# Optimization experiments

Hardware: AMD Instinct MI355X
Metric: run time of the kernel (lower is better)

Reference implementation:

```python
import jax, jax.numpy as jnp
import numpy as np
from jax.scipy.linalg import expm

S = 64          # alphabet size (codons)
M = 8           # number of models, prod(model_shape)
N_LEAVES = 32   # leaves of the balanced binary tree
N_EDGES = 62    # nodes 0..62, every non-root node has one parent edge (edge id == child node id)
B = 1024        # batch (alignment columns)
# per-level ranges of child-node ids; node 32+j has children (2j, 2j+1), etc.
LEVELS = [(0, 32), (32, 48), (48, 56), (56, 60), (60, 62)]


def inv_stereographic_projection(p):
    # maps R^{s-1} -> unit sphere S^{s-1}
    n2 = jnp.sum(p * p, axis=-1, keepdims=True)
    return jnp.concatenate([2.0 * p / (n2 + 1.0), (n2 - 1.0) / (n2 + 1.0)], axis=-1)


def generator(R, pi):
    # R: (M, s(s-1)/2) exchangeabilities, pi: (M, s) stationary distribution
    iu, ju = np.triu_indices(S, 1)
    A = jnp.zeros((M, S, S), R.dtype).at[:, iu, ju].set(R).at[:, ju, iu].set(R)
    Q = A * pi[:, None, :]                       # Q_ij = A_ij * pi_j (off-diagonal)
    row = jnp.sum(Q, axis=-1)                    # (M, S)
    return Q - jnp.eye(S, dtype=Q.dtype) * row[:, :, None]


def felsenstein(leave_configuration, R_inv, pi_inv, lengths):
    pi = inv_stereographic_projection(pi_inv) ** 2           # (M, S), rows sum to 1
    R = jnp.exp(R_inv)                                       # positive rates
    Q = generator(R, pi)                                     # (M, S, S)
    tQ = lengths[:, None, None, None] * Q[None]              # (E, M, S, S)
    P = jax.vmap(expm)(tQ.reshape(-1, S, S)).reshape(N_EDGES, M, S, S)
    # leaf alphas: tile leaf observations over the M models -> (n_leaves, B, M, S)
    prev = jnp.broadcast_to(
        leave_configuration.transpose(1, 0, 2)[:, :, None, :],
        (N_LEAVES, leave_configuration.shape[0], M, S))
    # level-synchronous pruning: messages up each parent edge, then product of the two children
    for a, b in LEVELS:
        msg = jnp.einsum('emcd,ebmd->ebmc', P[a:b], prev)    # per-edge transition
        prev = msg[0::2] * msg[1::2]                         # combine sibling pairs
    root = prev[0]                                           # (B, M, S)
    out = jnp.einsum('bms,ms->bm', root, pi)                 # P(data | model m)
    return out.reshape(out.shape[0], M)                      # (B, *model_shape)


def setup_inputs() -> dict:
    key = jax.random.key(0)
    k1, k2, k3, k4 = jax.random.split(key, 4)
    leave_configuration = jax.random.uniform(k1, (B, N_LEAVES, S), dtype=jnp.float32)
    tree_indices = jnp.zeros((B,), dtype=jnp.int32)          # single tree (F=1)
    R_inv = jax.random.uniform(k2, (M, S * (S - 1) // 2), dtype=jnp.float32,
                               minval=-1.0, maxval=1.0)
    pi_inv = jnp.full((M, S - 1), 1.0 / (np.sqrt(S) - 1.0), dtype=jnp.float32) \
        + 0.01 * jax.random.normal(k3, (M, S - 1), dtype=jnp.float32)
    lengths = jax.random.uniform(k4, (N_EDGES,), dtype=jnp.float32,
                                 minval=0.05, maxval=0.5)
    return {'leave_configuration': leave_configuration, 'R_inv': R_inv,
            'pi_inv': pi_inv, 'lengths': lengths, 'tree_indices': tree_indices}


def reference(leave_configuration, R_inv, pi_inv, lengths, tree_indices):
    # F=1: tf.dynamic_partition/gather_nd batch slicing is the identity, so
    # tree_indices is closed over / unused.
    return felsenstein(leave_configuration, R_inv, pi_inv, lengths)
```

## Files before the change

### kernel.cpp

```cpp
#include <hip/hip_runtime.h>

typedef unsigned short u16;
typedef unsigned int u32;
typedef __attribute__((ext_vector_type(8))) __bf16 bf16x8;
typedef __attribute__((ext_vector_type(4))) float f32x4;

constexpr int NM = 8;

constexpr size_t OFF_QP  = 0;
constexpr size_t OFF_PI  = 393216;
constexpr size_t OFF_PBH = 393728;
constexpr size_t OFF_PBL = OFF_PBH + 1015808;

union FR { uint4 u; bf16x8 v; };

__device__ __forceinline__ void split_bf16(float x, u16& h, u16& l) {
  u32 b = __float_as_uint(x);
  u32 hb = (b + 0x7fffu + ((b >> 16) & 1u)) & 0xffff0000u;
  h = (u16)(hb >> 16);
  float r = x - __uint_as_float(hb);
  l = (u16)(__float_as_uint(r) >> 16);
}

__device__ __forceinline__ void split8(const f32x4 a, const f32x4 b,
                                       uint4& hi, uint4& lo) {
  u16 h[8], l[8];
  split_bf16(a.x, h[0], l[0]); split_bf16(a.y, h[1], l[1]);
  split_bf16(a.z, h[2], l[2]); split_bf16(a.w, h[3], l[3]);
  split_bf16(b.x, h[4], l[4]); split_bf16(b.y, h[5], l[5]);
  split_bf16(b.z, h[6], l[6]); split_bf16(b.w, h[7], l[7]);
  hi.x = h[0] | ((u32)h[1] << 16); hi.y = h[2] | ((u32)h[3] << 16);
  hi.z = h[4] | ((u32)h[5] << 16); hi.w = h[6] | ((u32)h[7] << 16);
  lo.x = l[0] | ((u32)l[1] << 16); lo.y = l[2] | ((u32)l[3] << 16);
  lo.z = l[4] | ((u32)l[5] << 16); lo.w = l[6] | ((u32)l[7] << 16);
}

__device__ __forceinline__ void mfma3(f32x4& a, const uint4 ah, const uint4 al,
                                      const uint4 bh, const uint4 bl) {
  FR Ah, Al, Bh, Bl;
  Ah.u = ah; Al.u = al; Bh.u = bh; Bl.u = bl;
  a = __builtin_amdgcn_mfma_f32_16x16x32_bf16(Ah.v, Bh.v, a, 0, 0, 0);
  a = __builtin_amdgcn_mfma_f32_16x16x32_bf16(Ah.v, Bl.v, a, 0, 0, 0);
  a = __builtin_amdgcn_mfma_f32_16x16x32_bf16(Al.v, Bh.v, a, 0, 0, 0);
}

__device__ __forceinline__ void xt_read2(const u32* b, int row, int chunk,
                                         uint4& hi, uint4& lo) {
  const int dw = (row << 5) + (((chunk + row) & 7) << 2);
  hi = *(const uint4*)&b[dw];
  lo = *(const uint4*)&b[2048 + dw];
}
__device__ __forceinline__ void xt_write4(u32* b, int row, int cp, int half,
                                          const f32x4 v) {
  u16 h[4], l[4];
  split_bf16(v.x, h[0], l[0]); split_bf16(v.y, h[1], l[1]);
  split_bf16(v.z, h[2], l[2]); split_bf16(v.w, h[3], l[3]);
  const int dw = (row << 5) + (((cp + row) & 7) << 2) + half * 2;
  uint2 hh, ll;
  hh.x = h[0] | ((u32)h[1] << 16); hh.y = h[2] | ((u32)h[3] << 16);
  ll.x = l[0] | ((u32)l[1] << 16); ll.y = l[2] | ((u32)l[3] << 16);
  *(uint2*)&b[dw] = hh;
  *(uint2*)&b[2048 + dw] = ll;
}

__device__ void mmP(const u32* RX, const u32* CY, u32* dstC, u32* dstR,
                    float* __restrict__ g, int stid) {
  const int ln = stid & 15, kq = (stid >> 4) & 3, ct = stid >> 6;
  const f32x4 z = {0.f, 0.f, 0.f, 0.f};
  uint4 ah[2], al[2];
  #pragma unroll
  for (int kh = 0; kh < 2; ++kh)
    xt_read2(RX, ct * 16 + ln, kh * 4 + kq, ah[kh], al[kh]);
  f32x4 acc[4];
  #pragma unroll
  for (int bt = 0; bt < 4; ++bt) {
    acc[bt] = z;
    #pragma unroll
    for (int kh = 0; kh < 2; ++kh) {
      uint4 bh, bl;
      xt_read2(CY, bt * 16 + ln, kh * 4 + kq, bh, bl);
      mfma3(acc[bt], ah[kh], al[kh], bh, bl);
    }
  }
  #pragma unroll
  for (int bt = 0; bt < 4; ++bt) {
    #pragma unroll
    for (int r = 0; r < 4; ++r)
      g[(ct * 16 + kq * 4 + r) * 64 + bt * 16 + ln] = acc[bt][r];
    if (dstC) xt_write4(dstC, bt * 16 + ln, 2 * ct + (kq >> 1), kq & 1, acc[bt]);
  }
  if (dstR) {
    #pragma unroll
    for (int kh = 0; kh < 2; ++kh)
      xt_read2(CY, ct * 16 + ln, kh * 4 + kq, ah[kh], al[kh]);
    #pragma unroll
    for (int bt = 0; bt < 4; ++bt) {
      f32x4 a2 = z;
      #pragma unroll
      for (int kh = 0; kh < 2; ++kh) {
        uint4 bh, bl;
        xt_read2(RX, bt * 16 + ln, kh * 4 + kq, bh, bl);
        mfma3(a2, ah[kh], al[kh], bh, bl);
      }
      xt_write4(dstR, bt * 16 + ln, 2 * ct + (kq >> 1), kq & 1, a2);
    }
  }
}

__global__ __launch_bounds__(1024) void k_power(const float* __restrict__ R_inv,
                                                const float* __restrict__ pi_inv,
                                                float* __restrict__ ws) {
  const int m = blockIdx.x;
  const int tid = threadIdx.x;
  __shared__ float pis[64];
  __shared__ float n2s;
  __shared__ __align__(16) float Qs[64 * 68];
  __shared__ __align__(16) u32 PB[8][4096];
  if (tid < 64) {
    float p = (tid < 63) ? pi_inv[m * 63 + tid] : 0.f;
    float v = p * p;
    #pragma unroll
    for (int off = 32; off; off >>= 1) v += __shfl_down(v, off, 64);
    if (tid == 0) n2s = v;
  }
  __syncthreads();
  if (tid < 64) {
    const float den = n2s + 1.f;
    const float x = (tid < 63) ? 2.f * pi_inv[m * 63 + tid] / den
                               : (n2s - 1.f) / den;
    const float pv = x * x;
    pis[tid] = pv;
    ws[OFF_PI + (size_t)m * 64 + tid] = pv;
  }
  __syncthreads();
  for (int idx = tid; idx < 4096; idx += 1024) {
    const int i = idx >> 6, j = idx & 63;
    float q = 0.f;
    if (i != j) {
      const int a = min(i, j), b = max(i, j);
      const int kk = a * (127 - a) / 2 + (b - a - 1);
      q = expf(R_inv[m * 2016 + kk]) * pis[j];
    }
    Qs[i * 68 + j] = q;
  }
  __syncthreads();
  if (tid < 64) {
    float s = 0.f;
    #pragma unroll 4
    for (int j4 = 0; j4 < 64; j4 += 4) {
      const f32x4 q = *(const f32x4*)&Qs[tid * 68 + j4];
      s += q.x + q.y + q.z + q.w;
    }
    Qs[tid * 68 + tid] = -s;
  }
  __syncthreads();
  float* g1 = ws + OFF_QP + (size_t)m * 12 * 4096;
  for (int idx = tid; idx < 4096; idx += 1024)
    g1[idx] = Qs[(idx >> 6) * 68 + (idx & 63)];
  if (tid < 512) {
    const int i = tid >> 3, c = tid & 7;
    const f32x4 a = *(const f32x4*)&Qs[i * 68 + c * 8];
    const f32x4 b = *(const f32x4*)&Qs[i * 68 + c * 8 + 4];
    uint4 h, l;
    split8(a, b, h, l);
    const int dw = (i << 5) + (((c + i) & 7) << 2);
    *(uint4*)&PB[0][dw] = h;
    *(uint4*)&PB[0][2048 + dw] = l;
  } else {
    const int t2 = tid - 512, j = t2 >> 3, c = t2 & 7;
    f32x4 a, b;
    a.x = Qs[(c * 8 + 0) * 68 + j]; a.y = Qs[(c * 8 + 1) * 68 + j];
    a.z = Qs[(c * 8 + 2) * 68 + j]; a.w = Qs[(c * 8 + 3) * 68 + j];
    b.x = Qs[(c * 8 + 4) * 68 + j]; b.y = Qs[(c * 8 + 5) * 68 + j];
    b.z = Qs[(c * 8 + 6) * 68 + j]; b.w = Qs[(c * 8 + 7) * 68 + j];
    uint4 h, l;
    split8(a, b, h, l);
    const int dw = (j << 5) + (((c + j) & 7) << 2);
    *(uint4*)&PB[4][dw] = h;
    *(uint4*)&PB[4][2048 + dw] = l;
  }
  __syncthreads();
  const int sub = tid >> 8, stid = tid & 255;
  if (sub == 0) mmP(PB[0], PB[4], PB[5], PB[1], g1 + 4096, stid);
  __syncthreads();
  if (sub == 0) mmP(PB[1], PB[4], PB[6], nullptr, g1 + 2 * 4096, stid);
  else if (sub == 1) mmP(PB[1], PB[5], PB[7], PB[2], g1 + 3 * 4096, stid);
  __syncthreads();
  if (sub == 0) mmP(PB[2], PB[4], nullptr, nullptr, g1 + 4 * 4096, stid);
  else if (sub == 1) mmP(PB[2], PB[5], nullptr, nullptr, g1 + 5 * 4096, stid);
  else if (sub == 2) mmP(PB[2], PB[6], nullptr, nullptr, g1 + 6 * 4096, stid);
  else mmP(PB[2], PB[7], nullptr, PB[3], g1 + 7 * 4096, stid);
  __syncthreads();
  if (sub == 0) mmP(PB[3], PB[4], nullptr, nullptr, g1 + 8 * 4096, stid);
  else if (sub == 1) mmP(PB[3], PB[5], nullptr, nullptr, g1 + 9 * 4096, stid);
  else if (sub == 2) mmP(PB[3], PB[6], nullptr, nullptr, g1 + 10 * 4096, stid);
  else mmP(PB[3], PB[7], nullptr, nullptr, g1 + 11 * 4096, stid);
}

__global__ __launch_bounds__(256) void k_comb(const float* __restrict__ lengths,
                                              const float* __restrict__ ws,
                                              u16* __restrict__ ph_g,
                                              u16* __restrict__ pl_g) {
  const int e = blockIdx.x, m = blockIdx.y, tid = threadIdx.x;
  const float t = lengths[e];
  const float* qp = ws + OFF_QP + (size_t)m * 12 * 4096;
  u16* ph = ph_g + (((size_t)e * 8 + m) << 12);
  u16* pl = pl_g + (((size_t)e * 8 + m) << 12);
  float cf[12];
  cf[0] = t;
  #pragma unroll
  for (int k = 2; k <= 12; ++k) cf[k - 1] = cf[k - 2] * t / (float)k;
  #pragma unroll
  for (int rr = 0; rr < 4; ++rr) {
    const int off = rr * 1024 + tid * 4;
    const int i = off >> 6, j0 = off & 63;
    f32x4 a = {0.f, 0.f, 0.f, 0.f};
    if (i >= j0 && i < j0 + 4) a[i - j0] = 1.f;
    #pragma unroll
    for (int k = 1; k <= 12; ++k) {
      const f32x4 q = *(const f32x4*)&qp[(size_t)(k - 1) * 4096 + off];
      a += cf[k - 1] * q;
    }
    u16 h[4], l[4];
    split_bf16(a.x, h[0], l[0]); split_bf16(a.y, h[1], l[1]);
    split_bf16(a.z, h[2], l[2]); split_bf16(a.w, h[3], l[3]);
    ushort4 h4, l4;
    h4.x = h[0]; h4.y = h[1]; h4.z = h[2]; h4.w = h[3];
    l4.x = l[0]; l4.y = l[1]; l4.z = l[2]; l4.w = l[3];
    *(ushort4*)(ph + off) = h4;
    *(ushort4*)(pl + off) = l4;
  }
}

__global__ __launch_bounds__(1024) void k_tree(
    const float* __restrict__ leaves, const u16* __restrict__ Phi,
    const u16* __restrict__ Plo, const float* __restrict__ ws,
    float* __restrict__ out) {
  const int m = blockIdx.x & 7, btile = blockIdx.x >> 3;
  const int tid = threadIdx.x, lane = tid & 63, w = tid >> 6;
  const int ln = lane & 15, kq = lane >> 4;
  __shared__ __align__(16) float slots[16 * 2048];
  __shared__ float part[2][4][16];
  const f32x4 z = {0.f, 0.f, 0.f, 0.f};

  auto do_pair = [&](int p, int eb, int in0, int instr, int out_slot, int bt0,
                     int nbt, int ct0, int nct, bool leaf, f32x4* rootout) {
    uint4 bh[2][2], bl[2][2];
    f32x4 acc0[4][2];
    #pragma unroll
    for (int s = 0; s < 2; ++s) {
      #pragma unroll
      for (int bi = 0; bi < 2; ++bi) {
        if (bi >= nbt) continue;
        const int r = (bt0 + bi) * 16 + ln;
        #pragma unroll
        for (int kh = 0; kh < 2; ++kh) {
          f32x4 xa, xb;
          if (leaf) {
            const float* g = leaves + (size_t)(btile * 32 + r) * 2048 +
                             (size_t)(eb + 2 * p + s) * 64 + kh * 32 + kq * 8;
            xa = __builtin_nontemporal_load((const f32x4*)g);
            xb = __builtin_nontemporal_load((const f32x4*)(g + 4));
          } else {
            const float* nb = slots + (in0 + s * instr) * 2048 + r * 64;
            const int cj = kh * 8 + kq * 2;
            xa = *(const f32x4*)&nb[((cj + r) & 15) << 2];
            xb = *(const f32x4*)&nb[((cj + 1 + r) & 15) << 2];
          }
          split8(xa, xb, bh[bi][kh], bl[bi][kh]);
        }
      }
      const size_t pbase = ((size_t)(eb + 2 * p + s) * 8 + m) << 12;
      #pragma unroll
      for (int ci = 0; ci < 4; ++ci) {
        if (ci >= nct) continue;
        const int ct = ct0 + ci;
        uint4 ah[2], al[2];
        #pragma unroll
        for (int kh = 0; kh < 2; ++kh) {
          const size_t off = pbase + (size_t)(ct * 16 + ln) * 64 + kh * 32 + kq * 8;
          ah[kh] = *(const uint4*)(Phi + off);
          al[kh] = *(const uint4*)(Plo + off);
        }
        #pragma unroll
        for (int bi = 0; bi < 2; ++bi) {
          if (bi >= nbt) continue;
          f32x4 a = z;
          #pragma unroll
          for (int kh = 0; kh < 2; ++kh)
            mfma3(a, ah[kh], al[kh], bh[bi][kh], bl[bi][kh]);
          if (s == 0) {
            acc0[ci][bi] = a;
          } else {
            const f32x4 pr = acc0[ci][bi] * a;
            if (rootout) {
              *rootout = pr;
            } else {
              const int r = (bt0 + bi) * 16 + ln;
              float* nb = slots + out_slot * 2048 + r * 64;
              *(f32x4*)&nb[((ct * 4 + kq + r) & 15) << 2] = pr;
            }
          }
        }
      }
    }
  };

  do_pair(w, 0, 0, 0, w, 0, 2, 0, 4, true, nullptr);
  __syncthreads();
  do_pair(w >> 1, 32, (w >> 1) * 2, 1, (w >> 1) * 2, w & 1, 1, 0, 4, false,
          nullptr);
  __syncthreads();
  do_pair(w >> 2, 48, (w >> 2) * 4, 2, (w >> 2) * 4 + 1, w & 1, 1,
          ((w >> 1) & 1) * 2, 2, false, nullptr);
  __syncthreads();
  do_pair(w >> 3, 56, (w >> 3) * 8 + 1, 4, (w >> 3) * 8, w & 1, 1, (w >> 1) & 3,
          1, false, nullptr);
  __syncthreads();
  if (w < 8) {
    f32x4 prod = z;
    do_pair(0, 60, 0, 8, 0, w & 1, 1, w >> 1, 1, false, &prod);
    const f32x4 piv =
        *(const f32x4*)&ws[OFF_PI + (size_t)m * 64 + (w >> 1) * 16 + kq * 4];
    float v = prod.x * piv.x + prod.y * piv.y + prod.z * piv.z + prod.w * piv.w;
    v += __shfl_xor(v, 16, 64);
    v += __shfl_xor(v, 32, 64);
    if (lane < 16) part[w & 1][w >> 1][lane] = v;
  }
  __syncthreads();
  if (tid < 32) {
    const int bt = tid >> 4, bb = tid & 15;
    out[(size_t)(btile * 32 + tid) * 8 + m] =
        part[bt][0][bb] + part[bt][1][bb] + part[bt][2][bb] + part[bt][3][bb];
  }
}

extern "C" void kernel_launch(void* const* d_in, const int* in_sizes, int n_in,
                              void* d_out, int out_size, void* d_ws, size_t ws_size,
                              hipStream_t stream) {
  const float* leaves  = (const float*)d_in[0];
  const float* R_inv   = (const float*)d_in[1];
  const float* pi_inv  = (const float*)d_in[2];
  const float* lengths = (const float*)d_in[3];
  float* out = (float*)d_out;
  float* ws  = (float*)d_ws;

  u16* PBH = (u16*)(ws + OFF_PBH);
  u16* PBL = (u16*)(ws + OFF_PBL);

  hipLaunchKernelGGL(k_power, dim3(NM), dim3(1024), 0, stream, R_inv, pi_inv, ws);
  hipLaunchKernelGGL(k_comb, dim3(62, NM), dim3(256), 0, stream, lengths, ws,
                     PBH, PBL);
  hipLaunchKernelGGL(k_tree, dim3(256), dim3(1024), 0, stream, leaves, PBH, PBL,
                     ws, out);
}
```

Before: 132.6 us.

## Fuse power and combine kernels, store tree nodes as split bf16, halve tree block

The Q-power computation and the Taylor combination are merged into one kernel with 128 blocks. Each block recomputes all 12 powers of Q for its model, keeps them in registers and combines them for 4 edges, which removes the global round trip of the powers and one launch, at the cost of redundant power computation across 16 blocks per model. The tree kernel now uses 512 threads with two blocks per CU. It stores intermediate node vectors in shared memory as pre-split bf16 hi/lo pairs, so the split is no longer redone on every read, and it preloads both children's P fragments before issuing the MFMAs. Leaf loads switch from nontemporal to ordinary loads.

```diff
diff --git a/kernel.cpp b/kernel.cpp
--- a/kernel.cpp
+++ b/kernel.cpp
@@ -5,11 +5,8 @@
 typedef __attribute__((ext_vector_type(8))) __bf16 bf16x8;
 typedef __attribute__((ext_vector_type(4))) float f32x4;
 
-constexpr int NM = 8;
-
-constexpr size_t OFF_QP  = 0;
-constexpr size_t OFF_PI  = 393216;
-constexpr size_t OFF_PBH = 393728;
+constexpr size_t OFF_PI  = 0;
+constexpr size_t OFF_PBH = 512;
 constexpr size_t OFF_PBL = OFF_PBH + 1015808;
 
 union FR { uint4 u; bf16x8 v; };
@@ -63,59 +60,18 @@
   *(uint2*)&b[2048 + dw] = ll;
 }
 
-__device__ void mmP(const u32* RX, const u32* CY, u32* dstC, u32* dstR,
-                    float* __restrict__ g, int stid) {
-  const int ln = stid & 15, kq = (stid >> 4) & 3, ct = stid >> 6;
-  const f32x4 z = {0.f, 0.f, 0.f, 0.f};
-  uint4 ah[2], al[2];
-  #pragma unroll
-  for (int kh = 0; kh < 2; ++kh)
-    xt_read2(RX, ct * 16 + ln, kh * 4 + kq, ah[kh], al[kh]);
-  f32x4 acc[4];
-  #pragma unroll
-  for (int bt = 0; bt < 4; ++bt) {
-    acc[bt] = z;
-    #pragma unroll
-    for (int kh = 0; kh < 2; ++kh) {
-      uint4 bh, bl;
-      xt_read2(CY, bt * 16 + ln, kh * 4 + kq, bh, bl);
-      mfma3(acc[bt], ah[kh], al[kh], bh, bl);
-    }
-  }
-  #pragma unroll
-  for (int bt = 0; bt < 4; ++bt) {
-    #pragma unroll
-    for (int r = 0; r < 4; ++r)
-      g[(ct * 16 + kq * 4 + r) * 64 + bt * 16 + ln] = acc[bt][r];
-    if (dstC) xt_write4(dstC, bt * 16 + ln, 2 * ct + (kq >> 1), kq & 1, acc[bt]);
-  }
-  if (dstR) {
-    #pragma unroll
-    for (int kh = 0; kh < 2; ++kh)
-      xt_read2(CY, ct * 16 + ln, kh * 4 + kq, ah[kh], al[kh]);
-    #pragma unroll
-    for (int bt = 0; bt < 4; ++bt) {
-      f32x4 a2 = z;
-      #pragma unroll
-      for (int kh = 0; kh < 2; ++kh) {
-        uint4 bh, bl;
-        xt_read2(RX, bt * 16 + ln, kh * 4 + kq, bh, bl);
-        mfma3(a2, ah[kh], al[kh], bh, bl);
-      }
-      xt_write4(dstR, bt * 16 + ln, 2 * ct + (kq >> 1), kq & 1, a2);
-    }
-  }
-}
-
-__global__ __launch_bounds__(1024) void k_power(const float* __restrict__ R_inv,
-                                                const float* __restrict__ pi_inv,
-                                                float* __restrict__ ws) {
-  const int m = blockIdx.x;
-  const int tid = threadIdx.x;
+__global__ __launch_bounds__(1024) void k_pcomb(
+    const float* __restrict__ R_inv, const float* __restrict__ pi_inv,
+    const float* __restrict__ lengths, float* __restrict__ ws,
+    u16* __restrict__ PBH, u16* __restrict__ PBL) {
+  const int m = blockIdx.x & 7, prt = blockIdx.x >> 3;
+  const int tid = threadIdx.x, lane = tid & 63, w = tid >> 6;
+  const int ln = lane & 15, kq = lane >> 4;
   __shared__ float pis[64];
   __shared__ float n2s;
   __shared__ __align__(16) float Qs[64 * 68];
   __shared__ __align__(16) u32 PB[8][4096];
+
   if (tid < 64) {
     float p = (tid < 63) ? pi_inv[m * 63 + tid] : 0.f;
     float v = p * p;
@@ -130,7 +86,7 @@
                                : (n2s - 1.f) / den;
     const float pv = x * x;
     pis[tid] = pv;
-    ws[OFF_PI + (size_t)m * 64 + tid] = pv;
+    if (prt == 0) ws[OFF_PI + (size_t)m * 64 + tid] = pv;
   }
   __syncthreads();
   for (int idx = tid; idx < 4096; idx += 1024) {
@@ -154,9 +110,10 @@
     Qs[tid * 68 + tid] = -s;
   }
   __syncthreads();
-  float* g1 = ws + OFF_QP + (size_t)m * 12 * 4096;
-  for (int idx = tid; idx < 4096; idx += 1024)
-    g1[idx] = Qs[(idx >> 6) * 68 + (idx & 63)];
+  float q[12][4];
+  const int ci0 = tid >> 4, cj0 = (tid & 15) * 4;
+  #pragma unroll
+  for (int r = 0; r < 4; ++r) q[0][r] = Qs[ci0 * 68 + cj0 + r];
   if (tid < 512) {
     const int i = tid >> 3, c = tid & 7;
     const f32x4 a = *(const f32x4*)&Qs[i * 68 + c * 8];
@@ -180,158 +137,212 @@
     *(uint4*)&PB[4][2048 + dw] = l;
   }
   __syncthreads();
-  const int sub = tid >> 8, stid = tid & 255;
-  if (sub == 0) mmP(PB[0], PB[4], PB[5], PB[1], g1 + 4096, stid);
-  __syncthreads();
-  if (sub == 0) mmP(PB[1], PB[4], PB[6], nullptr, g1 + 2 * 4096, stid);
-  else if (sub == 1) mmP(PB[1], PB[5], PB[7], PB[2], g1 + 3 * 4096, stid);
-  __syncthreads();
-  if (sub == 0) mmP(PB[2], PB[4], nullptr, nullptr, g1 + 4 * 4096, stid);
-  else if (sub == 1) mmP(PB[2], PB[5], nullptr, nullptr, g1 + 5 * 4096, stid);
-  else if (sub == 2) mmP(PB[2], PB[6], nullptr, nullptr, g1 + 6 * 4096, stid);
-  else mmP(PB[2], PB[7], nullptr, PB[3], g1 + 7 * 4096, stid);
-  __syncthreads();
-  if (sub == 0) mmP(PB[3], PB[4], nullptr, nullptr, g1 + 8 * 4096, stid);
-  else if (sub == 1) mmP(PB[3], PB[5], nullptr, nullptr, g1 + 9 * 4096, stid);
-  else if (sub == 2) mmP(PB[3], PB[6], nullptr, nullptr, g1 + 10 * 4096, stid);
-  else mmP(PB[3], PB[7], nullptr, nullptr, g1 + 11 * 4096, stid);
-}
-
-__global__ __launch_bounds__(256) void k_comb(const float* __restrict__ lengths,
-                                              const float* __restrict__ ws,
-                                              u16* __restrict__ ph_g,
-                                              u16* __restrict__ pl_g) {
-  const int e = blockIdx.x, m = blockIdx.y, tid = threadIdx.x;
-  const float t = lengths[e];
-  const float* qp = ws + OFF_QP + (size_t)m * 12 * 4096;
-  u16* ph = ph_g + (((size_t)e * 8 + m) << 12);
-  u16* pl = pl_g + (((size_t)e * 8 + m) << 12);
-  float cf[12];
-  cf[0] = t;
+
+  const f32x4 z = {0.f, 0.f, 0.f, 0.f};
+  const int ct = w >> 2, bt = w & 3;
+  auto mm = [&](const u32* RX, const u32* CY, u32* dstC, u32* dstR) {
+    uint4 ah[2], al[2], bh[2], bl[2];
+    #pragma unroll
+    for (int kh = 0; kh < 2; ++kh) {
+      xt_read2(RX, ct * 16 + ln, kh * 4 + kq, ah[kh], al[kh]);
+      xt_read2(CY, bt * 16 + ln, kh * 4 + kq, bh[kh], bl[kh]);
+    }
+    f32x4 a = z;
+    #pragma unroll
+    for (int kh = 0; kh < 2; ++kh) mfma3(a, ah[kh], al[kh], bh[kh], bl[kh]);
+    #pragma unroll
+    for (int r = 0; r < 4; ++r)
+      Qs[(ct * 16 + kq * 4 + r) * 64 + bt * 16 + ln] = a[r];
+    if (dstC) xt_write4(dstC, bt * 16 + ln, 2 * ct + (kq >> 1), kq & 1, a);
+    if (dstR) {
+      #pragma unroll
+      for (int kh = 0; kh < 2; ++kh) {
+        xt_read2(CY, ct * 16 + ln, kh * 4 + kq, ah[kh], al[kh]);
+        xt_read2(RX, bt * 16 + ln, kh * 4 + kq, bh[kh], bl[kh]);
+      }
+      f32x4 a2 = z;
+      #pragma unroll
+      for (int kh = 0; kh < 2; ++kh) mfma3(a2, ah[kh], al[kh], bh[kh], bl[kh]);
+      xt_write4(dstR, bt * 16 + ln, 2 * ct + (kq >> 1), kq & 1, a2);
+    }
+  };
+  auto step = [&](const u32* RX, const u32* CY, int k, u32* dstC, u32* dstR) {
+    mm(RX, CY, dstC, dstR);
+    __syncthreads();
+    #pragma unroll
+    for (int r = 0; r < 4; ++r) q[k - 1][r] = Qs[tid * 4 + r];
+    __syncthreads();
+  };
+  step(PB[0], PB[4], 2, PB[5], PB[1]);
+  step(PB[1], PB[4], 3, PB[6], nullptr);
+  step(PB[1], PB[5], 4, PB[7], PB[2]);
+  step(PB[2], PB[4], 5, nullptr, nullptr);
+  step(PB[2], PB[5], 6, nullptr, nullptr);
+  step(PB[2], PB[6], 7, nullptr, nullptr);
+  step(PB[2], PB[7], 8, nullptr, PB[3]);
+  step(PB[3], PB[4], 9, nullptr, nullptr);
+  step(PB[3], PB[5], 10, nullptr, nullptr);
+  step(PB[3], PB[6], 11, nullptr, nullptr);
+  step(PB[3], PB[7], 12, nullptr, nullptr);
+
   #pragma unroll
-  for (int k = 2; k <= 12; ++k) cf[k - 1] = cf[k - 2] * t / (float)k;
-  #pragma unroll
-  for (int rr = 0; rr < 4; ++rr) {
-    const int off = rr * 1024 + tid * 4;
-    const int i = off >> 6, j0 = off & 63;
-    f32x4 a = {0.f, 0.f, 0.f, 0.f};
-    if (i >= j0 && i < j0 + 4) a[i - j0] = 1.f;
+  for (int ei = 0; ei < 4; ++ei) {
+    const int e = prt * 4 + ei;
+    if (e >= 62) break;
+    const float t = lengths[e];
+    float av[4] = {0.f, 0.f, 0.f, 0.f};
+    const int dr = ci0 - cj0;
+    if (dr >= 0 && dr < 4) av[dr] = 1.f;
+    float cf = 1.f;
     #pragma unroll
     for (int k = 1; k <= 12; ++k) {
-      const f32x4 q = *(const f32x4*)&qp[(size_t)(k - 1) * 4096 + off];
-      a += cf[k - 1] * q;
+      cf *= t / (float)k;
+      #pragma unroll
+      for (int r = 0; r < 4; ++r) av[r] = fmaf(cf, q[k - 1][r], av[r]);
     }
     u16 h[4], l[4];
-    split_bf16(a.x, h[0], l[0]); split_bf16(a.y, h[1], l[1]);
-    split_bf16(a.z, h[2], l[2]); split_bf16(a.w, h[3], l[3]);
+    split_bf16(av[0], h[0], l[0]); split_bf16(av[1], h[1], l[1]);
+    split_bf16(av[2], h[2], l[2]); split_bf16(av[3], h[3], l[3]);
+    const size_t base = (((size_t)e * 8 + m) << 12) + tid * 4;
     ushort4 h4, l4;
     h4.x = h[0]; h4.y = h[1]; h4.z = h[2]; h4.w = h[3];
     l4.x = l[0]; l4.y = l[1]; l4.z = l[2]; l4.w = l[3];
-    *(ushort4*)(ph + off) = h4;
-    *(ushort4*)(pl + off) = l4;
-  }
-}
-
-__global__ __launch_bounds__(1024) void k_tree(
+    *(ushort4*)(PBH + base) = h4;
+    *(ushort4*)(PBL + base) = l4;
+  }
+}
+
+__global__ __launch_bounds__(512, 2) void k_tree(
     const float* __restrict__ leaves, const u16* __restrict__ Phi,
     const u16* __restrict__ Plo, const float* __restrict__ ws,
     float* __restrict__ out) {
   const int m = blockIdx.x & 7, btile = blockIdx.x >> 3;
   const int tid = threadIdx.x, lane = tid & 63, w = tid >> 6;
   const int ln = lane & 15, kq = lane >> 4;
-  __shared__ __align__(16) float slots[16 * 2048];
-  __shared__ float part[2][4][16];
+  __shared__ __align__(16) u32 slots[16 * 2048];
+  __shared__ float psum[2][4][16];
   const f32x4 z = {0.f, 0.f, 0.f, 0.f};
 
-  auto do_pair = [&](int p, int eb, int in0, int instr, int out_slot, int bt0,
+  auto node_read = [&](int slot, int row, int kh, uint4& bh, uint4& bl) {
+    const int jc = kh * 8 + kq * 2;
+    const u32* b = &slots[slot * 2048 + row * 64];
+    const uint4 A = *(const uint4*)&b[((jc + row) & 15) << 2];
+    const uint4 B = *(const uint4*)&b[((jc + 1 + row) & 15) << 2];
+    bh.x = A.x; bh.y = A.y; bh.z = B.x; bh.w = B.y;
+    bl.x = A.z; bl.y = A.w; bl.z = B.z; bl.w = B.w;
+  };
+  auto node_write = [&](int slot, int row, int jc, const f32x4 v) {
+    u16 h[4], l[4];
+    split_bf16(v.x, h[0], l[0]); split_bf16(v.y, h[1], l[1]);
+    split_bf16(v.z, h[2], l[2]); split_bf16(v.w, h[3], l[3]);
+    uint4 pk;
+    pk.x = h[0] | ((u32)h[1] << 16); pk.y = h[2] | ((u32)h[3] << 16);
+    pk.z = l[0] | ((u32)l[1] << 16); pk.w = l[2] | ((u32)l[3] << 16);
+    *(uint4*)&slots[slot * 2048 + row * 64 + (((jc + row) & 15) << 2)] = pk;
+  };
+
+  auto do_pair = [&](int eb, int p, int s0, int s1, int outSlot, int bt0,
                      int nbt, int ct0, int nct, bool leaf, f32x4* rootout) {
-    uint4 bh[2][2], bl[2][2];
-    f32x4 acc0[4][2];
-    #pragma unroll
-    for (int s = 0; s < 2; ++s) {
+    uint4 bfh[2][2][2], bfl[2][2][2];
+    #pragma unroll
+    for (int s = 0; s < 2; ++s)
       #pragma unroll
       for (int bi = 0; bi < 2; ++bi) {
         if (bi >= nbt) continue;
-        const int r = (bt0 + bi) * 16 + ln;
+        const int row = (bt0 + bi) * 16 + ln;
         #pragma unroll
         for (int kh = 0; kh < 2; ++kh) {
-          f32x4 xa, xb;
           if (leaf) {
-            const float* g = leaves + (size_t)(btile * 32 + r) * 2048 +
+            const float* g = leaves + (size_t)(btile * 32 + row) * 2048 +
                              (size_t)(eb + 2 * p + s) * 64 + kh * 32 + kq * 8;
-            xa = __builtin_nontemporal_load((const f32x4*)g);
-            xb = __builtin_nontemporal_load((const f32x4*)(g + 4));
+            const f32x4 xa = *(const f32x4*)g;
+            const f32x4 xb = *(const f32x4*)(g + 4);
+            split8(xa, xb, bfh[s][bi][kh], bfl[s][bi][kh]);
           } else {
-            const float* nb = slots + (in0 + s * instr) * 2048 + r * 64;
-            const int cj = kh * 8 + kq * 2;
-            xa = *(const f32x4*)&nb[((cj + r) & 15) << 2];
-            xb = *(const f32x4*)&nb[((cj + 1 + r) & 15) << 2];
+            node_read(s ? s1 : s0, row, kh, bfh[s][bi][kh], bfl[s][bi][kh]);
           }
-          split8(xa, xb, bh[bi][kh], bl[bi][kh]);
         }
       }
-      const size_t pbase = ((size_t)(eb + 2 * p + s) * 8 + m) << 12;
+    uint4 ph[2][4][2], pl[2][4][2];
+    #pragma unroll
+    for (int s = 0; s < 2; ++s) {
+      const size_t pb = ((size_t)(eb + 2 * p + s) * 8 + m) << 12;
       #pragma unroll
       for (int ci = 0; ci < 4; ++ci) {
         if (ci >= nct) continue;
-        const int ct = ct0 + ci;
-        uint4 ah[2], al[2];
         #pragma unroll
         for (int kh = 0; kh < 2; ++kh) {
-          const size_t off = pbase + (size_t)(ct * 16 + ln) * 64 + kh * 32 + kq * 8;
-          ah[kh] = *(const uint4*)(Phi + off);
-          al[kh] = *(const uint4*)(Plo + off);
+          const size_t off =
+              pb + (size_t)((ct0 + ci) * 16 + ln) * 64 + kh * 32 + kq * 8;
+          ph[s][ci][kh] = *(const uint4*)(Phi + off);
+          pl[s][ci][kh] = *(const uint4*)(Plo + off);
         }
+      }
+    }
+    f32x4 a0[4][2];
+    #pragma unroll
+    for (int ci = 0; ci < 4; ++ci) {
+      if (ci >= nct) continue;
+      #pragma unroll
+      for (int bi = 0; bi < 2; ++bi) {
+        if (bi >= nbt) continue;
+        f32x4 a = z;
         #pragma unroll
-        for (int bi = 0; bi < 2; ++bi) {
-          if (bi >= nbt) continue;
-          f32x4 a = z;
-          #pragma unroll
-          for (int kh = 0; kh < 2; ++kh)
-            mfma3(a, ah[kh], al[kh], bh[bi][kh], bl[bi][kh]);
-          if (s == 0) {
-            acc0[ci][bi] = a;
-          } else {
-            const f32x4 pr = acc0[ci][bi] * a;
-            if (rootout) {
-              *rootout = pr;
-            } else {
-              const int r = (bt0 + bi) * 16 + ln;
-              float* nb = slots + out_slot * 2048 + r * 64;
-              *(f32x4*)&nb[((ct * 4 + kq + r) & 15) << 2] = pr;
-            }
-          }
-        }
-      }
-    }
-  };
-
-  do_pair(w, 0, 0, 0, w, 0, 2, 0, 4, true, nullptr);
-  __syncthreads();
-  do_pair(w >> 1, 32, (w >> 1) * 2, 1, (w >> 1) * 2, w & 1, 1, 0, 4, false,
-          nullptr);
-  __syncthreads();
-  do_pair(w >> 2, 48, (w >> 2) * 4, 2, (w >> 2) * 4 + 1, w & 1, 1,
-          ((w >> 1) & 1) * 2, 2, false, nullptr);
-  __syncthreads();
-  do_pair(w >> 3, 56, (w >> 3) * 8 + 1, 4, (w >> 3) * 8, w & 1, 1, (w >> 1) & 3,
-          1, false, nullptr);
-  __syncthreads();
-  if (w < 8) {
-    f32x4 prod = z;
-    do_pair(0, 60, 0, 8, 0, w & 1, 1, w >> 1, 1, false, &prod);
+        for (int kh = 0; kh < 2; ++kh)
+          mfma3(a, ph[0][ci][kh], pl[0][ci][kh], bfh[0][bi][kh], bfl[0][bi][kh]);
+        a0[ci][bi] = a;
+      }
+    }
+    #pragma unroll
+    for (int ci = 0; ci < 4; ++ci) {
+      if (ci >= nct) continue;
+      #pragma unroll
+      for (int bi = 0; bi < 2; ++bi) {
+        if (bi >= nbt) continue;
+        f32x4 a = z;
+        #pragma unroll
+        for (int kh = 0; kh < 2; ++kh)
+          mfma3(a, ph[1][ci][kh], pl[1][ci][kh], bfh[1][bi][kh], bfl[1][bi][kh]);
+        const f32x4 pr = a0[ci][bi] * a;
+        if (rootout)
+          *rootout = pr;
+        else
+          node_write(outSlot, (bt0 + bi) * 16 + ln, (ct0 + ci) * 4 + kq, pr);
+      }
+    }
+  };
+
+  do_pair(0, w, -1, -1, w, 0, 2, 0, 4, true, nullptr);
+  do_pair(0, w + 8, -1, -1, w + 8, 0, 2, 0, 4, true, nullptr);
+  __syncthreads();
+  do_pair(32, w, 2 * w, 2 * w + 1, 2 * w, 0, 2, 0, 4, false, nullptr);
+  __syncthreads();
+  {
+    const int j = w >> 1, bi = w & 1;
+    do_pair(48, j, 4 * j, 4 * j + 2, 4 * j, bi, 1, 0, 4, false, nullptr);
+  }
+  __syncthreads();
+  {
+    const int j = w >> 2, bi = w & 1, ch = (w >> 1) & 1;
+    do_pair(56, j, 8 * j, 8 * j + 4, 8 * j + 1, bi, 1, ch * 2, 2, false,
+            nullptr);
+  }
+  __syncthreads();
+  {
+    f32x4 pr = z;
+    do_pair(60, 0, 1, 9, -1, w & 1, 1, w >> 1, 1, false, &pr);
     const f32x4 piv =
         *(const f32x4*)&ws[OFF_PI + (size_t)m * 64 + (w >> 1) * 16 + kq * 4];
-    float v = prod.x * piv.x + prod.y * piv.y + prod.z * piv.z + prod.w * piv.w;
+    float v = pr.x * piv.x + pr.y * piv.y + pr.z * piv.z + pr.w * piv.w;
     v += __shfl_xor(v, 16, 64);
     v += __shfl_xor(v, 32, 64);
-    if (lane < 16) part[w & 1][w >> 1][lane] = v;
+    if (lane < 16) psum[w & 1][w >> 1][lane] = v;
   }
   __syncthreads();
   if (tid < 32) {
-    const int bt = tid >> 4, bb = tid & 15;
+    const int bi = tid >> 4, bb = tid & 15;
     out[(size_t)(btile * 32 + tid) * 8 + m] =
-        part[bt][0][bb] + part[bt][1][bb] + part[bt][2][bb] + part[bt][3][bb];
+        psum[bi][0][bb] + psum[bi][1][bb] + psum[bi][2][bb] + psum[bi][3][bb];
   }
 }
 
@@ -348,9 +359,8 @@
   u16* PBH = (u16*)(ws + OFF_PBH);
   u16* PBL = (u16*)(ws + OFF_PBL);
 
-  hipLaunchKernelGGL(k_power, dim3(NM), dim3(1024), 0, stream, R_inv, pi_inv, ws);
-  hipLaunchKernelGGL(k_comb, dim3(62, NM), dim3(256), 0, stream, lengths, ws,
-                     PBH, PBL);
-  hipLaunchKernelGGL(k_tree, dim3(256), dim3(1024), 0, stream, leaves, PBH, PBL,
+  hipLaunchKernelGGL(k_pcomb, dim3(128), dim3(1024), 0, stream, R_inv, pi_inv,
+                     lengths, ws, PBH, PBL);
+  hipLaunchKernelGGL(k_tree, dim3(256), dim3(512), 0, stream, leaves, PBH, PBL,
                      ws, out);
 }
```

Measured after the change: 124.5 us. 1.07x faster.
